# Kernel optimization log

Hardware: AMD Instinct MI355X
Metric: run time of the kernel (lower is better)

## Reference

```python
import jax, jax.numpy as jnp
import numpy as np

N = 50000      # nodes
E = 800000     # directed edges
IN = 64        # in_dim
ED = 16        # edge_dim
H = 8          # heads
D = 32         # hdim (per-head out channels)
NM = 500       # molecules (graphs)
SLOPE = 0.2    # GATConv negative_slope
MLP_SLOPE = 0.01  # torch LeakyReLU default in the Sequential


def _glorot(k, shape, fan_in):
    return jax.random.normal(k, shape, jnp.float32) * (1.0 / np.sqrt(fan_in))


def setup_inputs() -> dict:
    key = jax.random.key(0)
    ks = jax.random.split(key, 32)
    inp = {}
    inp["x"] = jax.random.normal(ks[0], (N, IN), jnp.float32)
    inp["edge_index"] = jax.random.randint(ks[1], (2, E), 0, N)
    inp["edge_attr"] = jax.random.normal(ks[2], (E, ED), jnp.float32)
    inp["batch"] = jnp.sort(jax.random.randint(ks[3], (N,), 0, NM))
    ins = [IN, H * D, H * D]
    i = 4
    for l in range(3):
        inp[f"W{l+1}"] = _glorot(ks[i], (ins[l], H * D), ins[l]); i += 1
        inp[f"as{l+1}"] = _glorot(ks[i], (H, D), D); i += 1
        inp[f"ad{l+1}"] = _glorot(ks[i], (H, D), D); i += 1
        inp[f"We{l+1}"] = _glorot(ks[i], (ED, H * D), ED); i += 1
        inp[f"ae{l+1}"] = _glorot(ks[i], (H, D), D); i += 1
        inp[f"b{l+1}"] = jnp.zeros((H * D,), jnp.float32); i += 1
    # final MLP: 4*H*D -> 3*D -> 2*D -> 1
    inp["lw1"] = _glorot(ks[i], (4 * H * D, 3 * D), 4 * H * D); i += 1
    inp["lb1"] = jnp.zeros((3 * D,), jnp.float32)
    inp["lw2"] = _glorot(ks[i], (3 * D, 2 * D), 3 * D); i += 1
    inp["lb2"] = jnp.zeros((2 * D,), jnp.float32)
    inp["lw3"] = _glorot(ks[i], (2 * D, 1), 2 * D); i += 1
    inp["lb3"] = jnp.zeros((1,), jnp.float32)
    return inp


def _gat_conv(x, src, dst, ea, W, a_s, a_d, We, a_e, b):
    n = x.shape[0]
    xl = (x @ W).reshape(n, H, D)           # [N,H,D]
    el = (ea @ We).reshape(-1, H, D)        # [E',H,D]
    a_src = jnp.einsum('nhd,hd->nh', xl, a_s)
    a_dst = jnp.einsum('nhd,hd->nh', xl, a_d)
    a_edg = jnp.einsum('ehd,hd->eh', el, a_e)
    alpha = a_src[src] + a_dst[dst] + a_edg         # [E',H]
    alpha = jax.nn.leaky_relu(alpha, SLOPE)
    amax = jax.ops.segment_max(alpha, dst, num_segments=n)
    ex = jnp.exp(alpha - amax[dst])
    den = jax.ops.segment_sum(ex, dst, num_segments=n)
    att = ex / den[dst]                              # segment softmax over dst
    msg = xl[src] * att[:, :, None]                  # [E',H,D]
    out = jax.ops.segment_sum(msg, dst, num_segments=n)
    return out.reshape(n, H * D) + b


def reference(x, edge_index, edge_attr, batch,
              W1, as1, ad1, We1, ae1, b1,
              W2, as2, ad2, We2, ae2, b2,
              W3, as3, ad3, We3, ae3, b3,
              lw1, lb1, lw2, lb2, lw3, lb3):
    n = x.shape[0]
    src0, dst0 = edge_index[0], edge_index[1]
    loop = jnp.arange(n)
    src = jnp.concatenate([src0, loop])
    dst = jnp.concatenate([dst0, loop])
    # fill_value='add': self-loop edge_attr = sum of incoming edge_attr per node
    ea_loop = jax.ops.segment_sum(edge_attr, dst0, num_segments=n)
    ea = jnp.concatenate([edge_attr, ea_loop], axis=0)

    h1 = _gat_conv(x, src, dst, ea, W1, as1, ad1, We1, ae1, b1)
    h2 = _gat_conv(h1, src, dst, ea, W2, as2, ad2, We2, ae2, b2)
    h3 = _gat_conv(h2, src, dst, ea, W3, as3, ad3, We3, ae3, b3)

    h_pool = jax.ops.segment_sum(h3, batch, num_segments=NM)
    h_pool_ = h_pool[batch]   # == repeat_interleave(h_pool, counts) for sorted batch
    h = jnp.concatenate([h1, h2, h3, h_pool_], axis=1)
    h = jax.nn.leaky_relu(h @ lw1 + lb1, MLP_SLOPE)
    h = jax.nn.leaky_relu(h @ lw2 + lb2, MLP_SLOPE)
    h = h @ lw3 + lb3
    return jax.nn.sigmoid(h)
```

## Files before the change

kernel.cpp:

```cpp
#include <hip/hip_runtime.h>
#include <hip/hip_bf16.h>

namespace {
constexpr int kN    = 50000;
constexpr int kE    = 800000;
constexpr int kEtot = kE + kN;
constexpr int kEd   = 16;
constexpr int kH    = 8;
constexpr int kD    = 32;
constexpr int kC    = kH * kD;
constexpr int kNM   = 500;
constexpr int kNB   = (kN + 255) / 256;
constexpr int kCap  = 128;
}

typedef __attribute__((ext_vector_type(8))) _Float16 half8;
typedef __attribute__((ext_vector_type(4))) float floatx4;

__device__ __forceinline__ float h2f(ushort u) {
  union { ushort u; _Float16 h; } v;
  v.u = u;
  return (float)v.h;
}
__device__ __forceinline__ ushort f2h(float f) {
  union { _Float16 h; ushort u; } v;
  v.h = (_Float16)f;
  return v.u;
}

__global__ void gat_zero2(int* __restrict__ a, int* __restrict__ b, int n) {
  int i = blockIdx.x * blockDim.x + threadIdx.x;
  if (i < n) { a[i] = 0; b[i] = 0; }
}

__global__ void gat_zeropad(ushort* __restrict__ c1h) {
  int i = blockIdx.x * blockDim.x + threadIdx.x;
  if (i >= kN * 4) return;
  int row = i >> 2, q = i & 3;
  uint4 z = {0u, 0u, 0u, 0u};
  *(uint4*)(c1h + (long)row * 128 + 96 + q * 8) = z;
}

__global__ void cvt_all(const float* __restrict__ x,
                        const float* __restrict__ W1, const float* __restrict__ W2,
                        const float* __restrict__ W3, const float* __restrict__ lw1,
                        const float* __restrict__ lw2,
                        ushort* __restrict__ xh, ushort* __restrict__ Wt1,
                        ushort* __restrict__ Wt2, ushort* __restrict__ Wt3,
                        ushort* __restrict__ lwt1, ushort* __restrict__ lwt2p) {
  int i = blockIdx.x * blockDim.x + threadIdx.x;
  if (i < kN * 64) { xh[i] = f2h(x[i]); return; }
  i -= kN * 64;
  if (i < 256 * 64) {
    int n = i >> 6, k = i & 63;
    Wt1[i] = f2h(W1[(long)k * 256 + n]);
    return;
  }
  i -= 256 * 64;
  if (i < 256 * 256) {
    int n = i >> 8, k = i & 255;
    Wt2[i] = f2h(W2[(long)k * 256 + n]);
    return;
  }
  i -= 256 * 256;
  if (i < 256 * 256) {
    int n = i >> 8, k = i & 255;
    Wt3[i] = f2h(W3[(long)k * 256 + n]);
    return;
  }
  i -= 256 * 256;
  if (i < 96 * 1024) {
    int n = i >> 10, k = i & 1023;
    lwt1[i] = f2h(lw1[(long)k * 96 + n]);
    return;
  }
  i -= 96 * 1024;
  if (i < 64 * 128) {
    int n = i >> 7, k = i & 127;
    lwt2p[i] = (k < 96) ? f2h(lw2[(long)k * 64 + n]) : (ushort)0;
    return;
  }
}

__global__ void gat_make_q3(const float* __restrict__ We1, const float* __restrict__ ae1,
                            const float* __restrict__ We2, const float* __restrict__ ae2,
                            const float* __restrict__ We3, const float* __restrict__ ae3,
                            float* __restrict__ Q3) {
  int t = threadIdx.x;
  if (t >= 384) return;
  int l = t >> 7, r = t & 127;
  const float* We = (l == 0) ? We1 : (l == 1) ? We2 : We3;
  const float* ae = (l == 0) ? ae1 : (l == 1) ? ae2 : ae3;
  int c = r >> 3, h = r & 7;
  float s = 0.f;
#pragma unroll
  for (int d = 0; d < kD; d++) s += We[c * kC + h * kD + d] * ae[h * kD + d];
  Q3[l * 128 + c * kH + h] = s;
}

__global__ void gat_count(const int* __restrict__ ei, int* __restrict__ deg) {
  int e = blockIdx.x * blockDim.x + threadIdx.x;
  if (e >= kE) return;
  atomicAdd(&deg[ei[kE + e]], 1);
}

__global__ __launch_bounds__(256) void gat_scan_a(const int* __restrict__ deg,
                                                  int* __restrict__ offs,
                                                  int* __restrict__ bsum) {
  __shared__ int s[256];
  int b = blockIdx.x, t = threadIdx.x;
  int i = b * 256 + t;
  int v = (i < kN) ? deg[i] + 1 : 0;
  s[t] = v;
  __syncthreads();
  for (int o = 1; o < 256; o <<= 1) {
    int u = (t >= o) ? s[t - o] : 0;
    __syncthreads();
    s[t] += u;
    __syncthreads();
  }
  if (i < kN) offs[i] = s[t] - v;
  if (t == 255) bsum[b] = s[255];
}

__global__ __launch_bounds__(256) void gat_scan_b(const int* __restrict__ bsum,
                                                  int* __restrict__ bpre) {
  __shared__ int s[256];
  int t = threadIdx.x;
  int v = (t < kNB) ? bsum[t] : 0;
  s[t] = v;
  __syncthreads();
  for (int o = 1; o < 256; o <<= 1) {
    int u = (t >= o) ? s[t - o] : 0;
    __syncthreads();
    s[t] += u;
    __syncthreads();
  }
  if (t < kNB) bpre[t] = s[t] - v;
}

__global__ void gat_scan_c(int* __restrict__ offs, const int* __restrict__ bpre) {
  int i = blockIdx.x * blockDim.x + threadIdx.x;
  if (i < kN) offs[i] += bpre[blockIdx.x];
  if (i == 0) offs[kN] = kEtot;
}

__global__ void gat_fill(const int* __restrict__ ei, const int* __restrict__ offs,
                         int* __restrict__ fillc, int* __restrict__ el,
                         int* __restrict__ esrc, int* __restrict__ epos) {
  int e = blockIdx.x * blockDim.x + threadIdx.x;
  if (e >= kEtot) return;
  int s, d;
  if (e < kE) { s = ei[e]; d = ei[kE + e]; }
  else { s = d = e - kE; }
  int pos = offs[d] + atomicAdd(&fillc[d], 1);
  el[pos] = e;
  esrc[pos] = s;
  epos[e] = pos;
}

__global__ __launch_bounds__(256) void gat_aq(const int* __restrict__ el,
                                              const float* __restrict__ ea,
                                              const float* __restrict__ Q3,
                                              float* __restrict__ aq0,
                                              float* __restrict__ aq1,
                                              float* __restrict__ aq2) {
  __shared__ float Qs[384];
  int t = threadIdx.x;
  for (int i = t; i < 384; i += 256) Qs[i] = Q3[i];
  __syncthreads();
  int pos = blockIdx.x * blockDim.x + t;
  if (pos >= kEtot) return;
  int e = el[pos];
  long base = (long)pos * kH;
  if (e >= kE) {
    float4 z = make_float4(0.f, 0.f, 0.f, 0.f);
    *(float4*)(aq0 + base) = z; *(float4*)(aq0 + base + 4) = z;
    *(float4*)(aq1 + base) = z; *(float4*)(aq1 + base + 4) = z;
    *(float4*)(aq2 + base) = z; *(float4*)(aq2 + base + 4) = z;
    return;
  }
  float eav[kEd];
#pragma unroll
  for (int q = 0; q < kEd / 4; q++) {
    float4 v = *(const float4*)(ea + (long)e * kEd + q * 4);
    eav[q * 4 + 0] = v.x; eav[q * 4 + 1] = v.y;
    eav[q * 4 + 2] = v.z; eav[q * 4 + 3] = v.w;
  }
  float* outp[3] = {aq0, aq1, aq2};
#pragma unroll
  for (int l = 0; l < 3; l++) {
    float av[kH];
#pragma unroll
    for (int h = 0; h < kH; h++) {
      float q = 0.f;
#pragma unroll
      for (int c = 0; c < kEd; c++) q += eav[c] * Qs[l * 128 + c * kH + h];
      av[h] = q;
    }
    *(float4*)(outp[l] + base) = make_float4(av[0], av[1], av[2], av[3]);
    *(float4*)(outp[l] + base + 4) = make_float4(av[4], av[5], av[6], av[7]);
  }
}

__global__ void gat_aqsum(const int* __restrict__ offs, const int* __restrict__ epos,
                          float* __restrict__ aq0, float* __restrict__ aq1,
                          float* __restrict__ aq2) {
  int t = blockIdx.x * blockDim.x + threadIdx.x;
  if (t >= kN * kH) return;
  int n = t >> 3, h = t & 7;
  int lo = offs[n], hi = offs[n + 1];
  float s0 = 0.f, s1 = 0.f, s2 = 0.f;
  for (int j = lo; j < hi; j++) {
    s0 += aq0[(long)j * kH + h];
    s1 += aq1[(long)j * kH + h];
    s2 += aq2[(long)j * kH + h];
  }
  long sp = (long)epos[kE + n] * kH + h;
  aq0[sp] = s0;
  aq1[sp] = s1;
  aq2[sp] = s2;
}

template <int AMODE, int COEF>
__global__ __launch_bounds__(256) void gat_gemm_mfma(
    int M, int K, int N,
    const ushort* __restrict__ A0, const ushort* __restrict__ A1,
    const ushort* __restrict__ A2, const ushort* __restrict__ A3,
    const int* __restrict__ batch,
    const ushort* __restrict__ Bt, const float* __restrict__ bias,
    float* __restrict__ C, int ldc, ushort* __restrict__ Ch, int ldch, int act,
    const float* __restrict__ as_, const float* __restrict__ ad_,
    float* __restrict__ a_src, float* __restrict__ a_dst) {
  __shared__ ushort As[8][64][8];
  __shared__ ushort Bs[8][128][8];
  int t = threadIdx.x;
  int rowBase = blockIdx.y * 64;
  int colBase = blockIdx.x * 128;
  int w = t >> 6, L = t & 63;

  floatx4 acc[8];
#pragma unroll
  for (int i = 0; i < 8; i++) acc[i] = (floatx4){0.f, 0.f, 0.f, 0.f};

  int ar = t >> 2, akq = t & 3;
  int arow = rowBase + ar;
  int bn = t >> 1, bq2 = (t & 1) * 4;
  int bok = (colBase + bn) < N;
  long brow = (long)(colBase + bn) * K;

  for (int k0 = 0; k0 < K; k0 += 64) {
#pragma unroll
    for (int half = 0; half < 2; half++) {
      int q = akq + half * 4;
      int gk = k0 + q * 8;
      uint4 av = {0u, 0u, 0u, 0u};
      if (arow < M) {
        if (AMODE == 0) {
          av = *(const uint4*)(A0 + (long)arow * K + gk);
        } else {
          int j = gk >> 8, kc = gk & 255;
          const ushort* src = (j == 0) ? A0 : (j == 1) ? A1 : (j == 2) ? A2 : A3;
          long rr = (j == 3) ? (long)batch[arow] : (long)arow;
          av = *(const uint4*)(src + rr * 256 + kc);
        }
      }
      *(uint4*)&As[q][ar][0] = av;
    }
#pragma unroll
    for (int u = 0; u < 4; u++) {
      int q = bq2 + u;
      uint4 bv = {0u, 0u, 0u, 0u};
      if (bok) bv = *(const uint4*)(Bt + brow + k0 + q * 8);
      *(uint4*)&Bs[q][bn][0] = bv;
    }
    __syncthreads();
    int mrow = w * 16 + (L & 15);
    int nl = L & 15;
#pragma unroll
    for (int half = 0; half < 2; half++) {
      int q = (L >> 4) + half * 4;
      half8 af = *(const half8*)&As[q][mrow][0];
#pragma unroll
      for (int t8 = 0; t8 < 8; t8++) {
        half8 bf = *(const half8*)&Bs[q][t8 * 16 + nl][0];
        acc[t8] = __builtin_amdgcn_mfma_f32_16x16x32_f16(af, bf, acc[t8], 0, 0, 0);
      }
    }
    __syncthreads();
  }
  int nlo = L & 15;
  int rbase = rowBase + w * 16 + (L >> 4) * 4;
#pragma unroll
  for (int t8 = 0; t8 < 8; t8++) {
    int col = colBase + t8 * 16 + nlo;
    if (col >= N) continue;
    float bv = bias ? bias[col] : 0.f;
#pragma unroll
    for (int r = 0; r < 4; r++) {
      int row = rbase + r;
      if (row >= M) continue;
      float v = acc[t8][r] + bv;
      if (act == 1) v = v > 0.f ? v : 0.01f * v;
      if (C) C[(long)row * ldc + col] = v;
      if (Ch) Ch[(long)row * ldch + col] = f2h(v);
    }
  }
  if (COEF) {
    float ps[4][4], pd[4][4];
#pragma unroll
    for (int g = 0; g < 4; g++)
#pragma unroll
      for (int r = 0; r < 4; r++) { ps[g][r] = 0.f; pd[g][r] = 0.f; }
    int hA = colBase >> 5;
#pragma unroll
    for (int t8 = 0; t8 < 8; t8++) {
      int g = t8 >> 1;
      int widx = (t8 & 1) * 16 + nlo;
      float wsv = as_[(hA + g) * kD + widx];
      float wdv = ad_[(hA + g) * kD + widx];
#pragma unroll
      for (int r = 0; r < 4; r++) {
        ps[g][r] += acc[t8][r] * wsv;
        pd[g][r] += acc[t8][r] * wdv;
      }
    }
#pragma unroll
    for (int m = 1; m < 16; m <<= 1) {
#pragma unroll
      for (int g = 0; g < 4; g++)
#pragma unroll
        for (int r = 0; r < 4; r++) {
          ps[g][r] += __shfl_xor(ps[g][r], m);
          pd[g][r] += __shfl_xor(pd[g][r], m);
        }
    }
    if (nlo == 0) {
#pragma unroll
      for (int r = 0; r < 4; r++) {
        int row = rbase + r;
        if (row >= M) continue;
#pragma unroll
        for (int g = 0; g < 4; g++) {
          a_src[row * kH + hA + g] = ps[g][r];
          a_dst[row * kH + hA + g] = pd[g][r];
        }
      }
    }
  }
}

__global__ __launch_bounds__(256) void gat_aggregate(
    const int* __restrict__ offs, const int* __restrict__ esrc,
    const float* __restrict__ aq,
    const float* __restrict__ a_src, const float* __restrict__ a_dst,
    const ushort* __restrict__ xlh, const float* __restrict__ bias,
    ushort* __restrict__ hh) {
  __shared__ float alf[4][kCap][kH];
  int wid = threadIdx.x >> 6;
  int n = blockIdx.x * 4 + wid;
  int L = threadIdx.x & 63;
  int lo = offs[n], hi = offs[n + 1];
  int deg = hi - lo;
  bool fits = (deg <= kCap);
  int hp = L & 7, sl = L >> 3;
  float adr = a_dst[n * kH + hp];
  float m = -1e30f;
  if (fits) {
    for (int j = lo + sl; j < hi; j += 8) {
      float a = a_src[esrc[j] * kH + hp] + adr + aq[(long)j * kH + hp];
      a = a > 0.f ? a : 0.2f * a;
      alf[wid][j - lo][hp] = a;
      m = fmaxf(m, a);
    }
  } else {
    for (int j = lo + sl; j < hi; j += 8) {
      float a = a_src[esrc[j] * kH + hp] + adr + aq[(long)j * kH + hp];
      a = a > 0.f ? a : 0.2f * a;
      m = fmaxf(m, a);
    }
  }
#pragma unroll
  for (int msk = 8; msk < 64; msk <<= 1) m = fmaxf(m, __shfl_xor(m, msk));
  __syncthreads();
  float s = 0.f;
  if (fits) {
    for (int j = lo + sl; j < hi; j += 8) {
      float pp = __expf(alf[wid][j - lo][hp] - m);
      alf[wid][j - lo][hp] = pp;
      s += pp;
    }
  } else {
    for (int j = lo + sl; j < hi; j += 8) {
      float a = a_src[esrc[j] * kH + hp] + adr + aq[(long)j * kH + hp];
      a = a > 0.f ? a : 0.2f * a;
      s += __expf(a - m);
    }
  }
#pragma unroll
  for (int msk = 8; msk < 64; msk <<= 1) s += __shfl_xor(s, msk);
  __syncthreads();
  int eh = L >> 5;
  int cl = L & 31;
  int c = cl * 8;
  int h = cl >> 2;
  float invs = 1.f / __shfl(s, h);
  float mh = __shfl(m, h);
  float acc[8] = {0.f, 0.f, 0.f, 0.f, 0.f, 0.f, 0.f, 0.f};
  union { uint4 u; _Float16 hf[8]; } v0, v1;
  if (fits) {
    int j = lo;
    for (; j + 4 <= hi; j += 4) {
      int jj0 = j + eh, jj1 = j + 2 + eh;
      int s0 = esrc[jj0], s1 = esrc[jj1];
      float t0 = alf[wid][jj0 - lo][h];
      float t1 = alf[wid][jj1 - lo][h];
      v0.u = *(const uint4*)(xlh + (long)s0 * kC + c);
      v1.u = *(const uint4*)(xlh + (long)s1 * kC + c);
#pragma unroll
      for (int i = 0; i < 8; i++) acc[i] += t0 * (float)v0.hf[i];
#pragma unroll
      for (int i = 0; i < 8; i++) acc[i] += t1 * (float)v1.hf[i];
    }
    for (; j < hi; j += 2) {
      int jj = j + eh;
      bool valid = jj < hi;
      int js = valid ? jj : lo;
      int sn = esrc[js];
      float att = valid ? alf[wid][jj - lo][h] : 0.f;
      v0.u = *(const uint4*)(xlh + (long)sn * kC + c);
#pragma unroll
      for (int i = 0; i < 8; i++) acc[i] += att * (float)v0.hf[i];
    }
  } else {
    float adh = a_dst[n * kH + h];
    for (int j = lo; j < hi; j += 2) {
      int jj = j + eh;
      bool valid = jj < hi;
      int js = valid ? jj : lo;
      int sn = esrc[js];
      float a = a_src[sn * kH + h] + adh + aq[(long)js * kH + h];
      a = a > 0.f ? a : 0.2f * a;
      float att = valid ? __expf(a - mh) : 0.f;
      v0.u = *(const uint4*)(xlh + (long)sn * kC + c);
#pragma unroll
      for (int i = 0; i < 8; i++) acc[i] += att * (float)v0.hf[i];
    }
  }
#pragma unroll
  for (int i = 0; i < 8; i++) acc[i] += __shfl_xor(acc[i], 32);
  if (eh == 0) {
    float4 b0 = *(const float4*)(bias + c);
    float4 b1 = *(const float4*)(bias + c + 4);
    ushort o[8];
    o[0] = f2h(acc[0] * invs + b0.x); o[1] = f2h(acc[1] * invs + b0.y);
    o[2] = f2h(acc[2] * invs + b0.z); o[3] = f2h(acc[3] * invs + b0.w);
    o[4] = f2h(acc[4] * invs + b1.x); o[5] = f2h(acc[5] * invs + b1.y);
    o[6] = f2h(acc[6] * invs + b1.z); o[7] = f2h(acc[7] * invs + b1.w);
    *(uint4*)(hh + (long)n * kC + c) = *(uint4*)o;
  }
}

__global__ __launch_bounds__(256) void gat_pool_seg(const ushort* __restrict__ h3h,
                                                    const int* __restrict__ batch,
                                                    ushort* __restrict__ hpoolh) {
  int m = blockIdx.x;
  int c = threadIdx.x;
  int lo = 0, hi = kN;
  while (lo < hi) { int mid = (lo + hi) >> 1; if (batch[mid] < m) lo = mid + 1; else hi = mid; }
  int start = lo;
  hi = kN;
  while (lo < hi) { int mid = (lo + hi) >> 1; if (batch[mid] < m + 1) lo = mid + 1; else hi = mid; }
  int end = lo;
  float s = 0.f;
  for (int n = start; n < end; n++) s += h2f(h3h[(long)n * kC + c]);
  hpoolh[(long)m * kC + c] = f2h(s);
}

__global__ void gat_mlp3(const float* __restrict__ c2, const float* __restrict__ lw3,
                         const float* __restrict__ lb3, float* __restrict__ out) {
  int n = blockIdx.x * blockDim.x + threadIdx.x;
  if (n >= kN) return;
  float s = lb3[0];
  const float* r = c2 + (long)n * 64;
#pragma unroll
  for (int k = 0; k < 64; k++) s += r[k] * lw3[k];
  float v = 1.f / (1.f + __expf(-s));
  out[n] = v;
}

static inline int cdiv(int a, int b) { return (a + b - 1) / b; }

extern "C" void kernel_launch(void* const* d_in, const int* in_sizes, int n_in,
                              void* d_out, int out_size, void* d_ws, size_t ws_size,
                              hipStream_t stream) {
  (void)in_sizes; (void)n_in; (void)out_size; (void)ws_size;
  const float* x = (const float*)d_in[0];
  const int* ei = (const int*)d_in[1];
  const float* ea = (const float*)d_in[2];
  const int* batch = (const int*)d_in[3];
  const float *W[3], *as_[3], *ad_[3], *We_[3], *ae_[3], *bb[3];
  for (int l = 0; l < 3; l++) {
    W[l]   = (const float*)d_in[4 + 6 * l];
    as_[l] = (const float*)d_in[5 + 6 * l];
    ad_[l] = (const float*)d_in[6 + 6 * l];
    We_[l] = (const float*)d_in[7 + 6 * l];
    ae_[l] = (const float*)d_in[8 + 6 * l];
    bb[l]  = (const float*)d_in[9 + 6 * l];
  }
  const float* lw1 = (const float*)d_in[22];
  const float* lb1 = (const float*)d_in[23];
  const float* lw2 = (const float*)d_in[24];
  const float* lb2 = (const float*)d_in[25];
  const float* lw3 = (const float*)d_in[26];
  const float* lb3 = (const float*)d_in[27];
  float* out = (float*)d_out;

  char* p = (char*)d_ws;
  auto carve = [&](size_t bytes) -> void* {
    void* r = (void*)p;
    p += (bytes + 255) & ~(size_t)255;
    return r;
  };
  float* aq0     = (float*)carve(sizeof(float) * (size_t)kEtot * kH);
  float* aq1     = (float*)carve(sizeof(float) * (size_t)kEtot * kH);
  float* aq2     = (float*)carve(sizeof(float) * (size_t)kEtot * kH);
  float* a_src   = (float*)carve(sizeof(float) * (size_t)kN * kH);
  float* a_dst   = (float*)carve(sizeof(float) * (size_t)kN * kH);
  float* Q3      = (float*)carve(sizeof(float) * 3 * 128);
  float* c2      = (float*)carve(sizeof(float) * (size_t)kN * 64);
  ushort* xh     = (ushort*)carve(sizeof(ushort) * (size_t)kN * 64);
  ushort* xlh    = (ushort*)carve(sizeof(ushort) * (size_t)kN * kC);
  ushort* h1h    = (ushort*)carve(sizeof(ushort) * (size_t)kN * kC);
  ushort* h2h    = (ushort*)carve(sizeof(ushort) * (size_t)kN * kC);
  ushort* h3h    = (ushort*)carve(sizeof(ushort) * (size_t)kN * kC);
  ushort* hpoolh = (ushort*)carve(sizeof(ushort) * (size_t)kNM * kC);
  ushort* Wt1    = (ushort*)carve(sizeof(ushort) * 64 * 256);
  ushort* Wt2    = (ushort*)carve(sizeof(ushort) * 256 * 256);
  ushort* Wt3    = (ushort*)carve(sizeof(ushort) * 256 * 256);
  ushort* lwt1   = (ushort*)carve(sizeof(ushort) * 1024 * 96);
  ushort* lwt2p  = (ushort*)carve(sizeof(ushort) * 64 * 128);
  int* deg   = (int*)carve(sizeof(int) * kN);
  int* fillc = (int*)carve(sizeof(int) * kN);
  int* offs  = (int*)carve(sizeof(int) * (kN + 1));
  int* bsum  = (int*)carve(sizeof(int) * 256);
  int* bpre  = (int*)carve(sizeof(int) * 256);
  int* el    = (int*)carve(sizeof(int) * kEtot);
  int* esrc  = (int*)carve(sizeof(int) * kEtot);
  int* epos  = (int*)carve(sizeof(int) * kEtot);
  ushort* c1h = (ushort*)aq0;

  gat_zero2<<<cdiv(kN, 256), 256, 0, stream>>>(deg, fillc, kN);
  {
    int tot = kN * 64 + 256 * 64 + 2 * 256 * 256 + 96 * 1024 + 64 * 128;
    cvt_all<<<cdiv(tot, 256), 256, 0, stream>>>(x, W[0], W[1], W[2], lw1, lw2,
                                                xh, Wt1, Wt2, Wt3, lwt1, lwt2p);
  }
  gat_make_q3<<<1, 384, 0, stream>>>(We_[0], ae_[0], We_[1], ae_[1], We_[2], ae_[2], Q3);

  gat_count<<<cdiv(kE, 256), 256, 0, stream>>>(ei, deg);
  gat_scan_a<<<kNB, 256, 0, stream>>>(deg, offs, bsum);
  gat_scan_b<<<1, 256, 0, stream>>>(bsum, bpre);
  gat_scan_c<<<kNB, 256, 0, stream>>>(offs, bpre);
  gat_fill<<<cdiv(kEtot, 256), 256, 0, stream>>>(ei, offs, fillc, el, esrc, epos);
  gat_aq<<<cdiv(kEtot, 256), 256, 0, stream>>>(el, ea, Q3, aq0, aq1, aq2);
  gat_aqsum<<<cdiv(kN * kH, 256), 256, 0, stream>>>(offs, epos, aq0, aq1, aq2);

  const ushort* hinh[3] = {xh, h1h, h2h};
  ushort* houth[3] = {h1h, h2h, h3h};
  const ushort* Wt[3] = {Wt1, Wt2, Wt3};
  const float* aqP[3] = {aq0, aq1, aq2};
  int kdim[3] = {64, kC, kC};
  for (int l = 0; l < 3; l++) {
    dim3 ggrid(kC / 128, cdiv(kN, 64));
    gat_gemm_mfma<0, 1><<<ggrid, 256, 0, stream>>>(
        kN, kdim[l], kC, hinh[l], nullptr, nullptr, nullptr, nullptr,
        Wt[l], nullptr, nullptr, 0, xlh, kC, 0,
        as_[l], ad_[l], a_src, a_dst);
    gat_aggregate<<<kN / 4, 256, 0, stream>>>(offs, esrc, aqP[l], a_src, a_dst,
                                              xlh, bb[l], houth[l]);
  }

  gat_pool_seg<<<kNM, kC, 0, stream>>>(h3h, batch, hpoolh);

  {
    gat_zeropad<<<cdiv(kN * 4, 256), 256, 0, stream>>>(c1h);
    dim3 g1(1, cdiv(kN, 64));
    gat_gemm_mfma<2, 0><<<g1, 256, 0, stream>>>(
        kN, 4 * kC, 96, h1h, h2h, h3h, hpoolh, batch,
        lwt1, lb1, nullptr, 0, c1h, 128, 1,
        nullptr, nullptr, nullptr, nullptr);
    dim3 g2(1, cdiv(kN, 64));
    gat_gemm_mfma<0, 0><<<g2, 256, 0, stream>>>(
        kN, 128, 64, c1h, nullptr, nullptr, nullptr, nullptr,
        lwt2p, lb2, c2, 64, nullptr, 0, 1,
        nullptr, nullptr, nullptr, nullptr);
    gat_mlp3<<<cdiv(kN, 256), 256, 0, stream>>>(c2, lw3, lb3, out);
  }
}
```

Before: 737.2 us.

## Store edge attention terms in fp16, cache sources in LDS, unroll aggregation

The per-edge attention contributions (aq0..aq2) are now stored as fp16 instead of fp32, which halves their write and read traffic in gat_aq, gat_aqsum and every aggregate pass. The aggregate kernel caches each node's source indices in shared memory during the score pass, so the gather loop reads them from LDS rather than global memory. The gather loop is also unrolled to four edges per lane-pair, and a launch-bounds occupancy hint is added. In exchange, the edge terms and their self-loop sums lose precision, and the extra LDS array and unrolling raise per-block resource use.

```diff
diff --git a/kernel.cpp b/kernel.cpp
--- a/kernel.cpp
+++ b/kernel.cpp
@@ -162,9 +162,9 @@
 __global__ __launch_bounds__(256) void gat_aq(const int* __restrict__ el,
                                               const float* __restrict__ ea,
                                               const float* __restrict__ Q3,
-                                              float* __restrict__ aq0,
-                                              float* __restrict__ aq1,
-                                              float* __restrict__ aq2) {
+                                              ushort* __restrict__ aq0,
+                                              ushort* __restrict__ aq1,
+                                              ushort* __restrict__ aq2) {
   __shared__ float Qs[384];
   int t = threadIdx.x;
   for (int i = t; i < 384; i += 256) Qs[i] = Q3[i];
@@ -174,10 +174,10 @@
   int e = el[pos];
   long base = (long)pos * kH;
   if (e >= kE) {
-    float4 z = make_float4(0.f, 0.f, 0.f, 0.f);
-    *(float4*)(aq0 + base) = z; *(float4*)(aq0 + base + 4) = z;
-    *(float4*)(aq1 + base) = z; *(float4*)(aq1 + base + 4) = z;
-    *(float4*)(aq2 + base) = z; *(float4*)(aq2 + base + 4) = z;
+    uint4 z = {0u, 0u, 0u, 0u};
+    *(uint4*)(aq0 + base) = z;
+    *(uint4*)(aq1 + base) = z;
+    *(uint4*)(aq2 + base) = z;
     return;
   }
   float eav[kEd];
@@ -187,39 +187,38 @@
     eav[q * 4 + 0] = v.x; eav[q * 4 + 1] = v.y;
     eav[q * 4 + 2] = v.z; eav[q * 4 + 3] = v.w;
   }
-  float* outp[3] = {aq0, aq1, aq2};
+  ushort* outp[3] = {aq0, aq1, aq2};
 #pragma unroll
   for (int l = 0; l < 3; l++) {
-    float av[kH];
+    union { uint4 u; ushort us[8]; } o;
 #pragma unroll
     for (int h = 0; h < kH; h++) {
       float q = 0.f;
 #pragma unroll
       for (int c = 0; c < kEd; c++) q += eav[c] * Qs[l * 128 + c * kH + h];
-      av[h] = q;
-    }
-    *(float4*)(outp[l] + base) = make_float4(av[0], av[1], av[2], av[3]);
-    *(float4*)(outp[l] + base + 4) = make_float4(av[4], av[5], av[6], av[7]);
+      o.us[h] = f2h(q);
+    }
+    *(uint4*)(outp[l] + base) = o.u;
   }
 }
 
 __global__ void gat_aqsum(const int* __restrict__ offs, const int* __restrict__ epos,
-                          float* __restrict__ aq0, float* __restrict__ aq1,
-                          float* __restrict__ aq2) {
+                          ushort* __restrict__ aq0, ushort* __restrict__ aq1,
+                          ushort* __restrict__ aq2) {
   int t = blockIdx.x * blockDim.x + threadIdx.x;
   if (t >= kN * kH) return;
   int n = t >> 3, h = t & 7;
   int lo = offs[n], hi = offs[n + 1];
   float s0 = 0.f, s1 = 0.f, s2 = 0.f;
   for (int j = lo; j < hi; j++) {
-    s0 += aq0[(long)j * kH + h];
-    s1 += aq1[(long)j * kH + h];
-    s2 += aq2[(long)j * kH + h];
+    s0 += h2f(aq0[(long)j * kH + h]);
+    s1 += h2f(aq1[(long)j * kH + h]);
+    s2 += h2f(aq2[(long)j * kH + h]);
   }
   long sp = (long)epos[kE + n] * kH + h;
-  aq0[sp] = s0;
-  aq1[sp] = s1;
-  aq2[sp] = s2;
+  aq0[sp] = f2h(s0);
+  aq1[sp] = f2h(s1);
+  aq2[sp] = f2h(s2);
 }
 
 template <int AMODE, int COEF>
@@ -350,13 +349,14 @@
   }
 }
 
-__global__ __launch_bounds__(256) void gat_aggregate(
+__global__ __launch_bounds__(256, 8) void gat_aggregate(
     const int* __restrict__ offs, const int* __restrict__ esrc,
-    const float* __restrict__ aq,
+    const ushort* __restrict__ aq,
     const float* __restrict__ a_src, const float* __restrict__ a_dst,
     const ushort* __restrict__ xlh, const float* __restrict__ bias,
     ushort* __restrict__ hh) {
   __shared__ float alf[4][kCap][kH];
+  __shared__ int srcs[4][kCap];
   int wid = threadIdx.x >> 6;
   int n = blockIdx.x * 4 + wid;
   int L = threadIdx.x & 63;
@@ -368,14 +368,16 @@
   float m = -1e30f;
   if (fits) {
     for (int j = lo + sl; j < hi; j += 8) {
-      float a = a_src[esrc[j] * kH + hp] + adr + aq[(long)j * kH + hp];
+      int sidx = esrc[j];
+      float a = a_src[sidx * kH + hp] + adr + h2f(aq[(long)j * kH + hp]);
       a = a > 0.f ? a : 0.2f * a;
       alf[wid][j - lo][hp] = a;
+      if (hp == 0) srcs[wid][j - lo] = sidx;
       m = fmaxf(m, a);
     }
   } else {
     for (int j = lo + sl; j < hi; j += 8) {
-      float a = a_src[esrc[j] * kH + hp] + adr + aq[(long)j * kH + hp];
+      float a = a_src[esrc[j] * kH + hp] + adr + h2f(aq[(long)j * kH + hp]);
       a = a > 0.f ? a : 0.2f * a;
       m = fmaxf(m, a);
     }
@@ -392,7 +394,7 @@
     }
   } else {
     for (int j = lo + sl; j < hi; j += 8) {
-      float a = a_src[esrc[j] * kH + hp] + adr + aq[(long)j * kH + hp];
+      float a = a_src[esrc[j] * kH + hp] + adr + h2f(aq[(long)j * kH + hp]);
       a = a > 0.f ? a : 0.2f * a;
       s += __expf(a - m);
     }
@@ -407,27 +409,38 @@
   float invs = 1.f / __shfl(s, h);
   float mh = __shfl(m, h);
   float acc[8] = {0.f, 0.f, 0.f, 0.f, 0.f, 0.f, 0.f, 0.f};
-  union { uint4 u; _Float16 hf[8]; } v0, v1;
+  union { uint4 u; _Float16 hf[8]; } v0, v1, v2, v3;
   if (fits) {
     int j = lo;
-    for (; j + 4 <= hi; j += 4) {
-      int jj0 = j + eh, jj1 = j + 2 + eh;
-      int s0 = esrc[jj0], s1 = esrc[jj1];
-      float t0 = alf[wid][jj0 - lo][h];
-      float t1 = alf[wid][jj1 - lo][h];
+    for (; j + 8 <= hi; j += 8) {
+      int j0 = j + eh, j1 = j + 2 + eh, j2 = j + 4 + eh, j3 = j + 6 + eh;
+      int s0 = srcs[wid][j0 - lo];
+      int s1 = srcs[wid][j1 - lo];
+      int s2 = srcs[wid][j2 - lo];
+      int s3 = srcs[wid][j3 - lo];
+      float t0 = alf[wid][j0 - lo][h];
+      float t1 = alf[wid][j1 - lo][h];
+      float t2 = alf[wid][j2 - lo][h];
+      float t3 = alf[wid][j3 - lo][h];
       v0.u = *(const uint4*)(xlh + (long)s0 * kC + c);
       v1.u = *(const uint4*)(xlh + (long)s1 * kC + c);
+      v2.u = *(const uint4*)(xlh + (long)s2 * kC + c);
+      v3.u = *(const uint4*)(xlh + (long)s3 * kC + c);
 #pragma unroll
       for (int i = 0; i < 8; i++) acc[i] += t0 * (float)v0.hf[i];
 #pragma unroll
       for (int i = 0; i < 8; i++) acc[i] += t1 * (float)v1.hf[i];
+#pragma unroll
+      for (int i = 0; i < 8; i++) acc[i] += t2 * (float)v2.hf[i];
+#pragma unroll
+      for (int i = 0; i < 8; i++) acc[i] += t3 * (float)v3.hf[i];
     }
     for (; j < hi; j += 2) {
       int jj = j + eh;
       bool valid = jj < hi;
-      int js = valid ? jj : lo;
-      int sn = esrc[js];
-      float att = valid ? alf[wid][jj - lo][h] : 0.f;
+      int idx = valid ? jj - lo : 0;
+      int sn = srcs[wid][idx];
+      float att = valid ? alf[wid][idx][h] : 0.f;
       v0.u = *(const uint4*)(xlh + (long)sn * kC + c);
 #pragma unroll
       for (int i = 0; i < 8; i++) acc[i] += att * (float)v0.hf[i];
@@ -439,7 +452,7 @@
       bool valid = jj < hi;
       int js = valid ? jj : lo;
       int sn = esrc[js];
-      float a = a_src[sn * kH + h] + adh + aq[(long)js * kH + h];
+      float a = a_src[sn * kH + h] + adh + h2f(aq[(long)js * kH + h]);
       a = a > 0.f ? a : 0.2f * a;
       float att = valid ? __expf(a - mh) : 0.f;
       v0.u = *(const uint4*)(xlh + (long)sn * kC + c);
@@ -522,9 +535,9 @@
     p += (bytes + 255) & ~(size_t)255;
     return r;
   };
-  float* aq0     = (float*)carve(sizeof(float) * (size_t)kEtot * kH);
-  float* aq1     = (float*)carve(sizeof(float) * (size_t)kEtot * kH);
-  float* aq2     = (float*)carve(sizeof(float) * (size_t)kEtot * kH);
+  ushort* aq0    = (ushort*)carve(sizeof(ushort) * (size_t)kEtot * kH);
+  ushort* aq1    = (ushort*)carve(sizeof(ushort) * (size_t)kEtot * kH);
+  ushort* aq2    = (ushort*)carve(sizeof(ushort) * (size_t)kEtot * kH);
   float* a_src   = (float*)carve(sizeof(float) * (size_t)kN * kH);
   float* a_dst   = (float*)carve(sizeof(float) * (size_t)kN * kH);
   float* Q3      = (float*)carve(sizeof(float) * 3 * 128);
@@ -548,7 +561,7 @@
   int* el    = (int*)carve(sizeof(int) * kEtot);
   int* esrc  = (int*)carve(sizeof(int) * kEtot);
   int* epos  = (int*)carve(sizeof(int) * kEtot);
-  ushort* c1h = (ushort*)aq0;
+  ushort* c1h = aq0;
 
   gat_zero2<<<cdiv(kN, 256), 256, 0, stream>>>(deg, fillc, kN);
   {
@@ -569,7 +582,7 @@
   const ushort* hinh[3] = {xh, h1h, h2h};
   ushort* houth[3] = {h1h, h2h, h3h};
   const ushort* Wt[3] = {Wt1, Wt2, Wt3};
-  const float* aqP[3] = {aq0, aq1, aq2};
+  const ushort* aqP[3] = {aq0, aq1, aq2};
   int kdim[3] = {64, kC, kC};
   for (int l = 0; l < 3; l++) {
     dim3 ggrid(kC / 128, cdiv(kN, 64));
```

Result: faster. 717.1 us (-2.7%).
